# Kernel tuning notes

Measured on AMD Instinct MI355X. Metric: run time of the kernel, lower is better.

Reference implementation:

```python
import jax, jax.numpy as jnp
import numpy as np

EPS = 1e-7        # keras backend epsilon
ALPHA = 0.25
GAMMA = 2.0
NEG_INF = -1e30

B, T, V, L = 256, 1024, 128, 64
BLANK = V - 1     # blank_index=-1 in tf ctc_loss_v2


def setup_inputs() -> dict:
    key = jax.random.key(0)
    k1, k2 = jax.random.split(key)
    y_pred = jax.random.uniform(k1, (B, T, V), dtype=jnp.float32)
    y_true = jax.random.randint(k2, (B, L), 0, V - 1, dtype=jnp.int32)
    return {"y_true": y_true, "y_pred": y_pred}


def _ctc_neg_log_lik(y_true, y_pred):
    """Standard CTC forward (alpha) DP in log space; full lengths T and L."""
    b, t, v = y_pred.shape
    l = y_true.shape[1]
    s = 2 * l + 1
    # tf ctc_loss_v2 log-softmaxes its logits; logits here are log(y_pred+eps)
    logp = jax.nn.log_softmax(jnp.log(y_pred + EPS), axis=-1)     # [B,T,V]
    # extended label sequence: blank, l1, blank, l2, ..., blank    [B,S]
    ext = jnp.full((b, s), BLANK, dtype=y_true.dtype)
    ext = ext.at[:, 1::2].set(y_true)
    # per-timestep log-probs of extended labels -> [T,B,S]
    lp_ext = jnp.take_along_axis(logp, ext[:, None, :], axis=2)   # [B,T,S]
    lp_ext = jnp.transpose(lp_ext, (1, 0, 2))                     # [T,B,S]
    # skip transition s-2 -> s allowed iff ext[s] != blank and ext[s] != ext[s-2]
    ext_sm2 = jnp.pad(ext[:, :-2], ((0, 0), (2, 0)), constant_values=BLANK)
    allow_skip = (ext != BLANK) & (ext != ext_sm2)                # [B,S]

    alpha0 = jnp.full((b, s), NEG_INF, dtype=logp.dtype)
    alpha0 = alpha0.at[:, 0].set(lp_ext[0, :, 0])
    alpha0 = alpha0.at[:, 1].set(lp_ext[0, :, 1])

    def step(alpha, lp_t):
        a0 = alpha
        a1 = jnp.pad(alpha[:, :-1], ((0, 0), (1, 0)), constant_values=NEG_INF)
        a2 = jnp.pad(alpha[:, :-2], ((0, 0), (2, 0)), constant_values=NEG_INF)
        a2 = jnp.where(allow_skip, a2, NEG_INF)
        m = jnp.maximum(jnp.maximum(a0, a1), a2)                  # stable LSE
        lse = m + jnp.log(jnp.exp(a0 - m) + jnp.exp(a1 - m) + jnp.exp(a2 - m))
        return lse + lp_t, None

    alphaT, _ = jax.lax.scan(step, alpha0, lp_ext[1:])
    log_lik = jnp.logaddexp(alphaT[:, -1], alphaT[:, -2])         # [B]
    return -log_lik


def reference(y_true, y_pred):
    loss = _ctc_neg_log_lik(y_true, y_pred)                       # [B]
    p = jnp.exp(-loss)
    focal = ALPHA * (1.0 - p) ** GAMMA * loss
    return jnp.mean(focal)
```

## Files before the change

### kernel.cpp

```cpp
#include <hip/hip_runtime.h>


#define EPSF 1e-7f

constexpr int Bb  = 256;
constexpr int Tt  = 1024;
constexpr int Vv  = 128;
constexpr int Ll  = 64;
constexpr int CH  = 32;
constexpr int NCH = Tt / CH;
constexpr int NPH = NCH + 1;
constexpr int NSEG = 8;

template <int Ctrl, int RowMask, int BankMask, bool BoundCtrl>
__device__ __forceinline__ float dppf(float x) {
    return __int_as_float(__builtin_amdgcn_update_dpp(
        0, __float_as_int(x), Ctrl, RowMask, BankMask, BoundCtrl));
}

__device__ __forceinline__ float half_sum(float x) {
    x += dppf<0x111, 0xf, 0xf, true>(x);
    x += dppf<0x112, 0xf, 0xf, true>(x);
    x += dppf<0x114, 0xf, 0xf, true>(x);
    x += dppf<0x118, 0xf, 0xf, true>(x);
    x += dppf<0x142, 0xa, 0xf, false>(x);
    return x;
}

__device__ __forceinline__ float wave_max63(float x) {
    x = fmaxf(x, dppf<0x111, 0xf, 0xf, true>(x));
    x = fmaxf(x, dppf<0x112, 0xf, 0xf, true>(x));
    x = fmaxf(x, dppf<0x114, 0xf, 0xf, true>(x));
    x = fmaxf(x, dppf<0x118, 0xf, 0xf, true>(x));
    x = fmaxf(x, dppf<0x142, 0xa, 0xf, false>(x));
    x = fmaxf(x, dppf<0x143, 0xc, 0xf, false>(x));
    return x;
}

__device__ __forceinline__ float bcast63(float x) {
    return __int_as_float(__builtin_amdgcn_readlane(__float_as_int(x), 63));
}

#define DO_STEP(QE, QB, CHK)                                                 \
    do {                                                                     \
        const float am1_ = dppf<0x138, 0xf, 0xf, true>(a_odd);               \
        const float ne_  = (a_even + am1_) * (QB);                           \
        const float no_  = fmaf(maskf, am1_, a_odd + a_even) * (QE);         \
        const float n1_  = (a128 + a_odd) * (QB);                            \
        a_even = ne_; a_odd = no_; a128 = n1_;                               \
        if (CHK) {                                                           \
            const float m_ = fmaxf(fmaxf(a_even, a_odd), a128);              \
            if (__all(m_ < 0x1p-75f)) {                                      \
                const float    wmax_  = bcast63(wave_max63(m_));             \
                const unsigned e_     = __float_as_uint(wmax_) >> 23;        \
                const float    scale_ = __uint_as_float((254u - e_) << 23);  \
                eacc += (int)e_ - 127;                                       \
                a_even *= scale_; a_odd *= scale_; a128 *= scale_;           \
            }                                                                \
        }                                                                    \
    } while (0)

__launch_bounds__(256)
__global__ void fused_kernel(const int* __restrict__ y_true,
                             const float* __restrict__ y_pred,
                             float* __restrict__ num_ws,
                             float* __restrict__ den_ws) {
    const int lane = threadIdx.x & 63;
    const int wv   = threadIdx.x >> 6;

    __shared__ float4 gt4[2 * (CH / 4) * 64];
    __shared__ float4 bk4[2 * (CH / 4)];
    __shared__ float  dpart[8];

    if (blockIdx.x >= Bb) {
        const int idx = blockIdx.x - Bb;
        const int b   = idx >> 3;
        const int seg = idx & (NSEG - 1);
        const float4* src4 =
            (const float4*)(y_pred + (size_t)b * Tt * Vv) +
            seg * (Tt / NSEG) * (Vv / 4);
        const int h   = 2 * wv + (lane >> 5);
        const int c32 = lane & 31;
        float ll = 0.0f;
#pragma unroll
        for (int k = 0; k < 16; ++k) {
            const int r = h + 8 * k;
            const float4 v = src4[r * 32 + c32];
            const float  s = half_sum(v.x + v.y + v.z + v.w);
            if (c32 == 31) ll += __log2f(s + (float)Vv * EPSF);
        }
        if (c32 == 31) dpart[h] = ll;
        __syncthreads();
        if (threadIdx.x == 0) {
            float s = dpart[0] + dpart[1] + dpart[2] + dpart[3] +
                      dpart[4] + dpart[5] + dpart[6] + dpart[7];
            den_ws[seg * Bb + b] = s;
        }
        return;
    }

    const int    b   = blockIdx.x;
    const float* ygl = y_pred + (size_t)b * Tt * Vv;
    const int    lab = y_true[b * Ll + lane];

    float a_even = 0.0f, a_odd = 0.0f, a128 = 0.0f, maskf = 0.0f;
    int   eacc = 0;
    if (wv == 0) {
        const int labp = __shfl_up(lab, 1);
        maskf  = (lane == 0 || lab != labp) ? 1.0f : 0.0f;
        a_even = (lane == 0) ? 1.0f : 0.0f;
    }

    for (int p = 0; p < NPH; ++p) {
        if (wv == 3) {
            if (p < NCH && lane < CH) {
                ((float*)(bk4 + (p & 1) * (CH / 4)))[lane] =
                    ygl[(p * CH + lane) * Vv + (Vv - 1)];
            }
        } else if (wv >= 1) {
            if (p < NCH) {
                const int    tg0 = (wv - 1) * (CH / 2);
                const float* src = ygl + p * CH * Vv;
                float* gtw = (float*)(gt4 + (p & 1) * (CH / 4) * 64);
#pragma unroll 8
                for (int j = 0; j < CH / 2; ++j) {
                    const int tl = tg0 + j;
                    gtw[(tl >> 2) * 256 + lane * 4 + (tl & 3)] =
                        src[tl * Vv + lab];
                }
            }
        } else {
            const int c = p - 1;
            if (c >= 0) {
                __builtin_amdgcn_s_setprio(1);
                const float4* gbf = gt4 + (c & 1) * (CH / 4) * 64;
                const float4* bbf = bk4 + (c & 1) * (CH / 4);
                float4 gA = gbf[0 * 64 + lane], gB = gbf[1 * 64 + lane];
                float4 bA = bbf[0],             bB = bbf[1];
#pragma unroll
                for (int i = 0; i < CH / 4; ++i) {
                    DO_STEP(gA.x + EPSF, bA.x + EPSF, false);
                    DO_STEP(gA.y + EPSF, bA.y + EPSF, false);
                    DO_STEP(gA.z + EPSF, bA.z + EPSF, false);
                    DO_STEP(gA.w + EPSF, bA.w + EPSF, (i & 3) == 3);
                    gA = gB; bA = bB;
                    if (i < CH / 4 - 2) {
                        gB = gbf[(i + 2) * 64 + lane];
                        bB = bbf[i + 2];
                    }
                }
                __builtin_amdgcn_s_setprio(0);
            }
        }
        __syncthreads();
    }

    if (wv == 0 && lane == 63) {
        const float tot = fmaxf(a128 + a_odd, 1e-37f);
        num_ws[b] = __log2f(tot) + (float)eacc;
    }
}

__global__ void finalize_kernel(const float* __restrict__ num_ws,
                                const float* __restrict__ den_ws,
                                float* __restrict__ out) {
    const int i    = threadIdx.x;
    const int lane = i & 63;
    const int wv   = i >> 6;

    float ds = 0.0f;
#pragma unroll
    for (int k = 0; k < NSEG; ++k) ds += den_ws[k * Bb + i];

    const float log2lik = num_ws[i] - ds;
    const float ln_lik  = 0.69314718055994530942f * log2lik;
    const float loss    = -ln_lik;
    const float pp      = __expf(ln_lik);
    const float om      = 1.0f - pp;
    float f = 0.25f * om * om * loss;

#pragma unroll
    for (int off = 32; off > 0; off >>= 1) f += __shfl_xor(f, off);

    __shared__ float red[4];
    if (lane == 0) red[wv] = f;
    __syncthreads();
    if (i == 0)
        out[0] = (red[0] + red[1] + red[2] + red[3]) * (1.0f / (float)Bb);
}

extern "C" void kernel_launch(void* const* d_in, const int* in_sizes, int n_in,
                              void* d_out, int out_size, void* d_ws, size_t ws_size,
                              hipStream_t stream) {
    const int*   y_true = (const int*)d_in[0];
    const float* y_pred = (const float*)d_in[1];
    float* num_ws = (float*)d_ws;
    float* den_ws = num_ws + Bb;

    fused_kernel<<<Bb + Bb * NSEG, 256, 0, stream>>>(y_true, y_pred,
                                                     num_ws, den_ws);
    finalize_kernel<<<1, 256, 0, stream>>>(num_ws, den_ws, (float*)d_out);
}
```

Measured before the change: 215.2 us.

## Split denominator into own kernel and stream DP inputs via global_load_lds

Splits the fused kernel into a separate denominator kernel and a DP kernel, launched back to back on the same stream. The DP kernel now gathers label and blank probabilities with direct global-to-LDS loads instead of register round trips. It also doubles the chunk size to 64 timesteps and software-pipelines the LDS reads into register batches, which halves the number of block barriers. The cost is that the two stages run serially, so the old overlap between the DP blocks and the denominator blocks is lost. It also adds a kernel launch and raises LDS and register use per DP block.

```diff
diff --git a/kernel.cpp b/kernel.cpp
--- a/kernel.cpp
+++ b/kernel.cpp
@@ -3,13 +3,13 @@
 
 #define EPSF 1e-7f
 
-constexpr int Bb  = 256;
-constexpr int Tt  = 1024;
-constexpr int Vv  = 128;
-constexpr int Ll  = 64;
-constexpr int CH  = 32;
-constexpr int NCH = Tt / CH;
-constexpr int NPH = NCH + 1;
+constexpr int Bb   = 256;
+constexpr int Tt   = 1024;
+constexpr int Vv   = 128;
+constexpr int Ll   = 64;
+constexpr int CH   = 64;
+constexpr int NCH  = Tt / CH;
+constexpr int NPH  = NCH + 1;
 constexpr int NSEG = 8;
 
 template <int Ctrl, int RowMask, int BankMask, bool BoundCtrl>
@@ -60,48 +60,98 @@
         }                                                                    \
     } while (0)
 
-__launch_bounds__(256)
-__global__ void fused_kernel(const int* __restrict__ y_true,
-                             const float* __restrict__ y_pred,
-                             float* __restrict__ num_ws,
+#define GL_LDS(GP, LP)                                                       \
+    __builtin_amdgcn_global_load_lds(                                        \
+        (const __attribute__((address_space(1))) unsigned int*)(GP),         \
+        (__attribute__((address_space(3))) unsigned int*)(LP), 4, 0, 0)
+
+#define CONS4(Q0, Q1, Q2, Q3, BF, LAST)                                      \
+    DO_STEP((Q0) + EPSF, BF.x + EPSF, false);                                \
+    DO_STEP((Q1) + EPSF, BF.y + EPSF, false);                                \
+    DO_STEP((Q2) + EPSF, BF.z + EPSF, false);                                \
+    DO_STEP((Q3) + EPSF, BF.w + EPSF, LAST);
+
+#define LOADA(TB)                                                            \
+    la0  = G[(TB + 0)  * 64 + lane]; la1  = G[(TB + 1)  * 64 + lane];        \
+    la2  = G[(TB + 2)  * 64 + lane]; la3  = G[(TB + 3)  * 64 + lane];        \
+    la4  = G[(TB + 4)  * 64 + lane]; la5  = G[(TB + 5)  * 64 + lane];        \
+    la6  = G[(TB + 6)  * 64 + lane]; la7  = G[(TB + 7)  * 64 + lane];        \
+    la8  = G[(TB + 8)  * 64 + lane]; la9  = G[(TB + 9)  * 64 + lane];        \
+    la10 = G[(TB + 10) * 64 + lane]; la11 = G[(TB + 11) * 64 + lane];        \
+    la12 = G[(TB + 12) * 64 + lane]; la13 = G[(TB + 13) * 64 + lane];        \
+    la14 = G[(TB + 14) * 64 + lane]; la15 = G[(TB + 15) * 64 + lane];        \
+    pa0 = BL[(TB) / 4 + 0]; pa1 = BL[(TB) / 4 + 1];                          \
+    pa2 = BL[(TB) / 4 + 2]; pa3 = BL[(TB) / 4 + 3];
+
+#define LOADB(TB)                                                            \
+    lb0  = G[(TB + 0)  * 64 + lane]; lb1  = G[(TB + 1)  * 64 + lane];        \
+    lb2  = G[(TB + 2)  * 64 + lane]; lb3  = G[(TB + 3)  * 64 + lane];        \
+    lb4  = G[(TB + 4)  * 64 + lane]; lb5  = G[(TB + 5)  * 64 + lane];        \
+    lb6  = G[(TB + 6)  * 64 + lane]; lb7  = G[(TB + 7)  * 64 + lane];        \
+    lb8  = G[(TB + 8)  * 64 + lane]; lb9  = G[(TB + 9)  * 64 + lane];        \
+    lb10 = G[(TB + 10) * 64 + lane]; lb11 = G[(TB + 11) * 64 + lane];        \
+    lb12 = G[(TB + 12) * 64 + lane]; lb13 = G[(TB + 13) * 64 + lane];        \
+    lb14 = G[(TB + 14) * 64 + lane]; lb15 = G[(TB + 15) * 64 + lane];        \
+    pb0 = BL[(TB) / 4 + 0]; pb1 = BL[(TB) / 4 + 1];                          \
+    pb2 = BL[(TB) / 4 + 2]; pb3 = BL[(TB) / 4 + 3];
+
+#define CONSA()                                                              \
+    CONS4(la0,  la1,  la2,  la3,  pa0, false)                                \
+    CONS4(la4,  la5,  la6,  la7,  pa1, false)                                \
+    CONS4(la8,  la9,  la10, la11, pa2, false)                                \
+    CONS4(la12, la13, la14, la15, pa3, true)
+
+#define CONSB()                                                              \
+    CONS4(lb0,  lb1,  lb2,  lb3,  pb0, false)                                \
+    CONS4(lb4,  lb5,  lb6,  lb7,  pb1, false)                                \
+    CONS4(lb8,  lb9,  lb10, lb11, pb2, false)                                \
+    CONS4(lb12, lb13, lb14, lb15, pb3, true)
+
+__launch_bounds__(256, 8)
+__global__ void denom_kernel(const float* __restrict__ y_pred,
                              float* __restrict__ den_ws) {
+    const int idx  = blockIdx.x;
+    const int b    = idx >> 3;
+    const int seg  = idx & (NSEG - 1);
     const int lane = threadIdx.x & 63;
     const int wv   = threadIdx.x >> 6;
 
-    __shared__ float4 gt4[2 * (CH / 4) * 64];
-    __shared__ float4 bk4[2 * (CH / 4)];
-    __shared__ float  dpart[8];
-
-    if (blockIdx.x >= Bb) {
-        const int idx = blockIdx.x - Bb;
-        const int b   = idx >> 3;
-        const int seg = idx & (NSEG - 1);
-        const float4* src4 =
-            (const float4*)(y_pred + (size_t)b * Tt * Vv) +
-            seg * (Tt / NSEG) * (Vv / 4);
-        const int h   = 2 * wv + (lane >> 5);
-        const int c32 = lane & 31;
-        float ll = 0.0f;
-#pragma unroll
-        for (int k = 0; k < 16; ++k) {
-            const int r = h + 8 * k;
-            const float4 v = src4[r * 32 + c32];
-            const float  s = half_sum(v.x + v.y + v.z + v.w);
-            if (c32 == 31) ll += __log2f(s + (float)Vv * EPSF);
-        }
-        if (c32 == 31) dpart[h] = ll;
-        __syncthreads();
-        if (threadIdx.x == 0) {
-            float s = dpart[0] + dpart[1] + dpart[2] + dpart[3] +
-                      dpart[4] + dpart[5] + dpart[6] + dpart[7];
-            den_ws[seg * Bb + b] = s;
-        }
-        return;
-    }
-
-    const int    b   = blockIdx.x;
+    const float4* src4 =
+        (const float4*)(y_pred + (size_t)b * Tt * Vv) +
+        seg * (Tt / NSEG) * (Vv / 4);
+    const int h   = 2 * wv + (lane >> 5);
+    const int c32 = lane & 31;
+    float ll = 0.0f;
+#pragma unroll
+    for (int k = 0; k < 16; ++k) {
+        const int r = h + 8 * k;
+        const float4 v = src4[r * 32 + c32];
+        const float  s = half_sum(v.x + v.y + v.z + v.w);
+        if (c32 == 31) ll += __log2f(s + (float)Vv * EPSF);
+    }
+    __shared__ float dpart[8];
+    if (c32 == 31) dpart[h] = ll;
+    __syncthreads();
+    if (threadIdx.x == 0) {
+        den_ws[seg * Bb + b] = dpart[0] + dpart[1] + dpart[2] + dpart[3] +
+                               dpart[4] + dpart[5] + dpart[6] + dpart[7];
+    }
+}
+
+__launch_bounds__(256, 1)
+__global__ void dp_kernel(const int* __restrict__ y_true,
+                          const float* __restrict__ y_pred,
+                          float* __restrict__ num_ws) {
+    const int b    = blockIdx.x;
+    const int lane = threadIdx.x & 63;
+    const int wv   = threadIdx.x >> 6;
+
     const float* ygl = y_pred + (size_t)b * Tt * Vv;
-    const int    lab = y_true[b * Ll + lane];
+
+    __shared__ float garr[2 * CH * 64];
+    __shared__ float lblk[2 * CH];
+
+    const int lab = y_true[b * Ll + lane];
 
     float a_even = 0.0f, a_odd = 0.0f, a128 = 0.0f, maskf = 0.0f;
     int   eacc = 0;
@@ -112,45 +162,38 @@
     }
 
     for (int p = 0; p < NPH; ++p) {
-        if (wv == 3) {
-            if (p < NCH && lane < CH) {
-                ((float*)(bk4 + (p & 1) * (CH / 4)))[lane] =
-                    ygl[(p * CH + lane) * Vv + (Vv - 1)];
+        if (wv >= 1) {
+            if (p < NCH) {
+                const int    buf = p & 1;
+                const float* src = ygl + p * CH * Vv;
+                float*       dst = garr + buf * CH * 64;
+#pragma unroll
+                for (int j = 0; j < 22; ++j) {
+                    const int t = (wv - 1) + 3 * j;
+                    if (t < CH) GL_LDS(src + t * Vv + lab, dst + t * 64);
+                }
+                if (wv == 2)
+                    GL_LDS(src + lane * Vv + (Vv - 1), lblk + buf * CH);
             }
-        } else if (wv >= 1) {
-            if (p < NCH) {
-                const int    tg0 = (wv - 1) * (CH / 2);
-                const float* src = ygl + p * CH * Vv;
-                float* gtw = (float*)(gt4 + (p & 1) * (CH / 4) * 64);
-#pragma unroll 8
-                for (int j = 0; j < CH / 2; ++j) {
-                    const int tl = tg0 + j;
-                    gtw[(tl >> 2) * 256 + lane * 4 + (tl & 3)] =
-                        src[tl * Vv + lab];
-                }
-            }
-        } else {
-            const int c = p - 1;
-            if (c >= 0) {
-                __builtin_amdgcn_s_setprio(1);
-                const float4* gbf = gt4 + (c & 1) * (CH / 4) * 64;
-                const float4* bbf = bk4 + (c & 1) * (CH / 4);
-                float4 gA = gbf[0 * 64 + lane], gB = gbf[1 * 64 + lane];
-                float4 bA = bbf[0],             bB = bbf[1];
-#pragma unroll
-                for (int i = 0; i < CH / 4; ++i) {
-                    DO_STEP(gA.x + EPSF, bA.x + EPSF, false);
-                    DO_STEP(gA.y + EPSF, bA.y + EPSF, false);
-                    DO_STEP(gA.z + EPSF, bA.z + EPSF, false);
-                    DO_STEP(gA.w + EPSF, bA.w + EPSF, (i & 3) == 3);
-                    gA = gB; bA = bB;
-                    if (i < CH / 4 - 2) {
-                        gB = gbf[(i + 2) * 64 + lane];
-                        bB = bbf[i + 2];
-                    }
-                }
-                __builtin_amdgcn_s_setprio(0);
-            }
+        } else if (p > 0) {
+            const int     buf = (p - 1) & 1;
+            const float*  G   = garr + buf * CH * 64;
+            const float4* BL  = (const float4*)(lblk + buf * CH);
+            __builtin_amdgcn_s_setprio(1);
+            float la0, la1, la2, la3, la4, la5, la6, la7;
+            float la8, la9, la10, la11, la12, la13, la14, la15;
+            float lb0, lb1, lb2, lb3, lb4, lb5, lb6, lb7;
+            float lb8, lb9, lb10, lb11, lb12, lb13, lb14, lb15;
+            float4 pa0, pa1, pa2, pa3, pb0, pb1, pb2, pb3;
+            LOADA(0)
+            LOADB(16)
+            CONSA()
+            LOADA(32)
+            CONSB()
+            LOADB(48)
+            CONSA()
+            CONSB()
+            __builtin_amdgcn_s_setprio(0);
         }
         __syncthreads();
     }
@@ -197,7 +240,7 @@
     float* num_ws = (float*)d_ws;
     float* den_ws = num_ws + Bb;
 
-    fused_kernel<<<Bb + Bb * NSEG, 256, 0, stream>>>(y_true, y_pred,
-                                                     num_ws, den_ws);
+    denom_kernel<<<Bb * NSEG, 256, 0, stream>>>(y_pred, den_ws);
+    dp_kernel<<<Bb, 256, 0, stream>>>(y_true, y_pred, num_ws);
     finalize_kernel<<<1, 256, 0, stream>>>(num_ws, den_ws, (float*)d_out);
 }
```

Measured after the change: 222.5 us. 3.4% more time.
